# Optimization experiments

Measured on AMD Instinct MI355X. Metric: run time of the kernel, lower is better.

The kernel has to match this reference:

```python
import jax, jax.numpy as jnp
import numpy as np

B, IN_DIM, HID, LAT, L, K = 65536, 512, 256, 64, 3, 2048


def setup_inputs() -> dict:
    key = jax.random.key(0)
    ks = jax.random.split(key, 10)
    s = 0.05
    return {
        "x": jax.random.normal(ks[0], (B, IN_DIM), jnp.float32),
        "enc_w1": jax.random.normal(ks[1], (IN_DIM, HID), jnp.float32) * s,
        "enc_b1": jnp.zeros((HID,), jnp.float32),
        "enc_w2": jax.random.normal(ks[2], (HID, LAT), jnp.float32) * s,
        "enc_b2": jnp.zeros((LAT,), jnp.float32),
        "codebooks": jax.random.normal(ks[3], (L, K, LAT), jnp.float32),
        "dec_w1": jax.random.normal(ks[4], (LAT, HID), jnp.float32) * s,
        "dec_b1": jnp.zeros((HID,), jnp.float32),
        "dec_w2": jax.random.normal(ks[5], (HID, IN_DIM), jnp.float32) * s,
        "dec_b2": jnp.zeros((IN_DIM,), jnp.float32),
    }


def reference(x, enc_w1, enc_b1, enc_w2, enc_b2, codebooks,
              dec_w1, dec_b1, dec_w2, dec_b2):
    # encoder: Linear -> ReLU -> Linear
    z = jax.nn.relu(x @ enc_w1 + enc_b1) @ enc_w2 + enc_b2  # [B, LAT]

    quantized = jnp.zeros_like(z)
    codes, residuals = [], []
    num_layers = codebooks.shape[0]
    for i in range(num_layers):  # small fixed layer loop (structurally sequential)
        residual = z - jax.lax.stop_gradient(quantized)  # [B, LAT]
        residuals.append(residual)
        C = codebooks[i]  # [K, LAT]
        # squared euclidean distances (argmin identical to cdist argmin)
        sqdist = (jnp.sum(residual * residual, axis=-1, keepdims=True)
                  - 2.0 * (residual @ C.T)
                  + jnp.sum(C * C, axis=-1))  # [B, K]
        code = jnp.argmin(sqdist, axis=-1)  # [B]
        codes.append(code)
        quantized = C[code] + jax.lax.stop_gradient(quantized)

    # decoder: Linear -> ReLU -> Linear
    x_recon = jax.nn.relu(quantized @ dec_w1 + dec_b1) @ dec_w2 + dec_b2  # [B, IN_DIM]
    return (jnp.stack(codes), x_recon, quantized, jnp.stack(residuals))
```

## Files before the change

### kernel.cpp

```cpp
#include <hip/hip_runtime.h>
#include <float.h>

#define NB      65536
#define IN_DIM  512
#define HID     256
#define LAT     64
#define NLAYERS 3
#define NK      2048
#define DELTA   1e-2f

typedef __attribute__((ext_vector_type(8)))  short s16x8;
typedef __attribute__((ext_vector_type(16))) float fp32x16;

__device__ __forceinline__ unsigned short f2bf(float v) {
  unsigned u = __float_as_uint(v);
  unsigned r = (u + 0x7fffu + ((u >> 16) & 1u)) >> 16;
  return (unsigned short)r;
}
__device__ __forceinline__ float bf2f(unsigned short h) {
  return __uint_as_float((unsigned)h << 16);
}

template<bool RELU>
__global__ __launch_bounds__(256) void gemm_f32(
    const float* __restrict__ A, const float* __restrict__ W,
    const float* __restrict__ bias, float* __restrict__ C,
    int M, int N, int K) {
  __shared__ float As[32][132];
  __shared__ float Bs[32][64];
  const int tid = threadIdx.x;
  const int cg  = tid & 15;
  const int rg  = tid >> 4;
  const int m0  = blockIdx.x * 128;
  const int n0  = blockIdx.y * 64;

  float acc[8][4];
#pragma unroll
  for (int i = 0; i < 8; ++i)
#pragma unroll
    for (int j = 0; j < 4; ++j) acc[i][j] = 0.f;

  for (int k0 = 0; k0 < K; k0 += 32) {
#pragma unroll
    for (int p = 0; p < 4; ++p) {
      int a = tid + p * 256;
      int row = a >> 3, kq = (a & 7) * 4;
      float4 v = *reinterpret_cast<const float4*>(&A[(size_t)(m0 + row) * K + k0 + kq]);
      As[kq + 0][row] = v.x; As[kq + 1][row] = v.y;
      As[kq + 2][row] = v.z; As[kq + 3][row] = v.w;
    }
#pragma unroll
    for (int p = 0; p < 2; ++p) {
      int a = tid + p * 256;
      int kk = a >> 4, nq = (a & 15) * 4;
      *reinterpret_cast<float4*>(&Bs[kk][nq]) =
          *reinterpret_cast<const float4*>(&W[(size_t)(k0 + kk) * N + n0 + nq]);
    }
    __syncthreads();
#pragma unroll
    for (int kk = 0; kk < 32; ++kk) {
      float4 a0 = *reinterpret_cast<const float4*>(&As[kk][rg * 8]);
      float4 a1 = *reinterpret_cast<const float4*>(&As[kk][rg * 8 + 4]);
      float4 b0 = *reinterpret_cast<const float4*>(&Bs[kk][cg * 4]);
      float av[8] = {a0.x, a0.y, a0.z, a0.w, a1.x, a1.y, a1.z, a1.w};
      float bv[4] = {b0.x, b0.y, b0.z, b0.w};
#pragma unroll
      for (int i = 0; i < 8; ++i)
#pragma unroll
        for (int j = 0; j < 4; ++j)
          acc[i][j] = fmaf(av[i], bv[j], acc[i][j]);
    }
    __syncthreads();
  }

  float4 bb = *reinterpret_cast<const float4*>(&bias[n0 + cg * 4]);
  float bv[4] = {bb.x, bb.y, bb.z, bb.w};
#pragma unroll
  for (int i = 0; i < 8; ++i) {
    float vals[4];
#pragma unroll
    for (int j = 0; j < 4; ++j) {
      float v = __fadd_rn(acc[i][j], bv[j]);
      if (RELU) v = fmaxf(v, 0.f);
      vals[j] = v;
    }
    float4 o; o.x = vals[0]; o.y = vals[1]; o.z = vals[2]; o.w = vals[3];
    *reinterpret_cast<float4*>(&C[(size_t)(m0 + rg * 8 + i) * N + n0 + cg * 4]) = o;
  }
}

template<bool RELU>
__global__ __launch_bounds__(256) void gemm128(
    const float* __restrict__ A, const float* __restrict__ W,
    const float* __restrict__ bias, float* __restrict__ C,
    int M, int N, int K) {
  __shared__ float As[16][132];
  __shared__ float Bs[16][132];
  const int tid  = threadIdx.x;
  const int cg   = tid & 15;
  const int rg   = tid >> 4;
  const int sw   = (cg >> 2) & 1;
  const int colA = cg * 8 + sw * 4;
  const int colB = cg * 8 + (sw ^ 1) * 4;
  const int m0   = blockIdx.x * 128;
  const int n0   = blockIdx.y * 128;

  const int arow = tid >> 2;
  const int akq  = (tid & 3) * 4;
  const int bk   = tid >> 5;
  const int bn   = (tid & 31) * 4;

  const float* Ap0 = A + (size_t)(m0 + arow) * K + akq;
  const float* Ap1 = A + (size_t)(m0 + arow + 64) * K + akq;
  const float* Wp0 = W + (size_t)bk * N + n0 + bn;
  const float* Wp1 = W + (size_t)(bk + 8) * N + n0 + bn;

  float acc[8][8];
#pragma unroll
  for (int i = 0; i < 8; ++i)
#pragma unroll
    for (int j = 0; j < 8; ++j) acc[i][j] = 0.f;

  float4 av0, av1, bv0, bv1;
  av0 = *reinterpret_cast<const float4*>(Ap0);
  av1 = *reinterpret_cast<const float4*>(Ap1);
  bv0 = *reinterpret_cast<const float4*>(Wp0);
  bv1 = *reinterpret_cast<const float4*>(Wp1);

  auto write_tile = [&]() {
    As[akq + 0][arow] = av0.x; As[akq + 1][arow] = av0.y;
    As[akq + 2][arow] = av0.z; As[akq + 3][arow] = av0.w;
    As[akq + 0][arow + 64] = av1.x; As[akq + 1][arow + 64] = av1.y;
    As[akq + 2][arow + 64] = av1.z; As[akq + 3][arow + 64] = av1.w;
    *reinterpret_cast<float4*>(&Bs[bk][bn])     = bv0;
    *reinterpret_cast<float4*>(&Bs[bk + 8][bn]) = bv1;
  };
  auto compute_tile = [&]() {
#pragma unroll
    for (int kk = 0; kk < 16; ++kk) {
      float4 a0 = *reinterpret_cast<const float4*>(&As[kk][rg * 8]);
      float4 a1 = *reinterpret_cast<const float4*>(&As[kk][rg * 8 + 4]);
      float4 b0 = *reinterpret_cast<const float4*>(&Bs[kk][colA]);
      float4 b1 = *reinterpret_cast<const float4*>(&Bs[kk][colB]);
      float rv[8] = {a0.x, a0.y, a0.z, a0.w, a1.x, a1.y, a1.z, a1.w};
      float cv[8] = {b0.x, b0.y, b0.z, b0.w, b1.x, b1.y, b1.z, b1.w};
#pragma unroll
      for (int i = 0; i < 8; ++i)
#pragma unroll
        for (int j = 0; j < 8; ++j)
          acc[i][j] = fmaf(rv[i], cv[j], acc[i][j]);
    }
  };

  write_tile();
  __syncthreads();
#pragma unroll 1
  for (int k0 = 16; k0 < K; k0 += 16) {
    av0 = *reinterpret_cast<const float4*>(Ap0 + k0);
    av1 = *reinterpret_cast<const float4*>(Ap1 + k0);
    bv0 = *reinterpret_cast<const float4*>(Wp0 + (size_t)k0 * N);
    bv1 = *reinterpret_cast<const float4*>(Wp1 + (size_t)k0 * N);
    compute_tile();
    __syncthreads();
    write_tile();
    __syncthreads();
  }
  compute_tile();

  float4 bA = *reinterpret_cast<const float4*>(&bias[n0 + colA]);
  float4 bB = *reinterpret_cast<const float4*>(&bias[n0 + colB]);
  float ba[8] = {bA.x, bA.y, bA.z, bA.w, bB.x, bB.y, bB.z, bB.w};
#pragma unroll
  for (int i = 0; i < 8; ++i) {
    size_t row = (size_t)(m0 + rg * 8 + i);
    float o[8];
#pragma unroll
    for (int j = 0; j < 8; ++j) {
      float v = __fadd_rn(acc[i][j], ba[j]);
      if (RELU) v = fmaxf(v, 0.f);
      o[j] = v;
    }
    float4 oA; oA.x = o[0]; oA.y = o[1]; oA.z = o[2]; oA.w = o[3];
    float4 oB; oB.x = o[4]; oB.y = o[5]; oB.z = o[6]; oB.w = o[7];
    *reinterpret_cast<float4*>(&C[row * N + n0 + colA]) = oA;
    *reinterpret_cast<float4*>(&C[row * N + n0 + colB]) = oB;
  }
}

__global__ void cnorm_f32(const float* __restrict__ cb, float* __restrict__ cn) {
  int i = blockIdx.x * blockDim.x + threadIdx.x;
  if (i >= NLAYERS * NK) return;
  const float* row = cb + (size_t)i * LAT;
  float r[8];
#pragma unroll
  for (int j = 0; j < 8; ++j) r[j] = 0.f;
#pragma unroll
  for (int t = 0; t < 8; ++t)
#pragma unroll
    for (int j = 0; j < 8; ++j) {
      float v = row[t * 8 + j];
      r[j] = __fadd_rn(r[j], __fmul_rn(v, v));
    }
  cn[i] = __fadd_rn(__fadd_rn(__fadd_rn(r[0], r[1]), __fadd_rn(r[2], r[3])),
                    __fadd_rn(__fadd_rn(r[4], r[5]), __fadd_rn(r[6], r[7])));
}

__global__ void split_cb(const float* __restrict__ cb,
                         unsigned short* __restrict__ cbf) {
  const int sid  = blockIdx.x * 256 + threadIdx.x;
  const int lane = sid & 63;
  const int grp  = sid >> 6;
  const int fg   = grp & 7;
  const int chl  = grp >> 3;
  const int nt = fg >> 2, ks = fg & 3;
  const int layer = chl >> 5, ch = chl & 31;
  const int code = ch * 64 + nt * 32 + (lane & 31);
  const int k0 = ks * 16 + (lane >> 5) * 8;
  const float* src = cb + ((size_t)layer * NK + code) * LAT + k0;
  float4 a = *(const float4*)src;
  float4 b = *(const float4*)(src + 4);
  float v[8] = {a.x, a.y, a.z, a.w, b.x, b.y, b.z, b.w};
  s16x8 hi, lo;
#pragma unroll
  for (int i = 0; i < 8; ++i) {
    unsigned short h = f2bf(v[i]);
    hi[i] = (short)h;
    lo[i] = (short)f2bf(__fsub_rn(v[i], bf2f(h)));
  }
  *(s16x8*)(cbf + ((size_t)grp * 2 + 0) * 512 + lane * 8) = hi;
  *(s16x8*)(cbf + ((size_t)grp * 2 + 1) * 512 + lane * 8) = lo;
}

__global__ void split_w(const float* __restrict__ W,
                        unsigned short* __restrict__ wf, int K, int N) {
  const int total = (K / 16) * (N / 32) * 64;
  const int idx = blockIdx.x * 256 + threadIdx.x;
  if (idx >= total) return;
  const int lane = idx & 63;
  const int grp  = idx >> 6;
  const int ntn  = N / 32;
  const int ks   = grp / ntn;
  const int ntg  = grp % ntn;
  const int col  = ntg * 32 + (lane & 31);
  const int k0   = ks * 16 + (lane >> 5) * 8;
  s16x8 hi, lo;
#pragma unroll
  for (int i = 0; i < 8; ++i) {
    float v = W[(size_t)(k0 + i) * N + col];
    unsigned short h = f2bf(v);
    hi[i] = (short)h;
    lo[i] = (short)f2bf(__fsub_rn(v, bf2f(h)));
  }
  *(s16x8*)(wf + ((size_t)grp * 2 + 0) * 512 + lane * 8) = hi;
  *(s16x8*)(wf + ((size_t)grp * 2 + 1) * 512 + lane * 8) = lo;
}

__global__ __launch_bounds__(256, 2) void rq_mfma(
    const float* __restrict__ zg,
    const float* __restrict__ cb,
    const unsigned short* __restrict__ cbf,
    const float* __restrict__ cnorm,
    float* __restrict__ out_codes,
    float* __restrict__ out_quant,
    float* __restrict__ out_res) {
  __shared__ float m1S[64][4];
  __shared__ int   candS[64][16];
  __shared__ int   cntS[64][4];
  __shared__ int   flagS[64][4];
  __shared__ int   selS[64];
  __shared__ float rnS[64];
  __shared__ float bestD[256];
  __shared__ int   bestK[256];

  const int tid  = threadIdx.x;
  const int w    = tid >> 6;
  const int lane = tid & 63;
  const int half = lane >> 5;
  const int lcol = lane & 31;
  const int rb0  = blockIdx.x * 64;

  s16x8 ah[2][4], al[2][4];

  for (int layer = 0; layer < NLAYERS; ++layer) {
    const float* cbL = cb + (size_t)layer * NK * LAT;
    const float* cnL = cnorm + (size_t)layer * NK;
    const unsigned short* cbfL = cbf + (size_t)layer * (NK * LAT * 2);
    float* resL = out_res + (size_t)layer * NB * LAT;

#pragma unroll
    for (int m = 0; m < 2; ++m) {
      const size_t row = (size_t)(rb0 + m * 32 + lcol);
#pragma unroll
      for (int ks = 0; ks < 4; ++ks) {
        const int k0 = ks * 16 + half * 8;
        const float* zp = zg + row * LAT + k0;
        float4 a = *(const float4*)zp;
        float4 b = *(const float4*)(zp + 4);
        float r[8] = {a.x, a.y, a.z, a.w, b.x, b.y, b.z, b.w};
        if (layer > 0) {
          const float* qp = out_quant + row * LAT + k0;
          float4 qa = *(const float4*)qp;
          float4 qb = *(const float4*)(qp + 4);
          float q[8] = {qa.x, qa.y, qa.z, qa.w, qb.x, qb.y, qb.z, qb.w};
#pragma unroll
          for (int i = 0; i < 8; ++i) r[i] = __fsub_rn(r[i], q[i]);
          if (w == 0) {
            float4 o0 = {r[0], r[1], r[2], r[3]};
            float4 o1 = {r[4], r[5], r[6], r[7]};
            *(float4*)(resL + row * LAT + k0) = o0;
            *(float4*)(resL + row * LAT + k0 + 4) = o1;
          }
        }
#pragma unroll
        for (int i = 0; i < 8; ++i) {
          unsigned short hh = f2bf(r[i]);
          float hf = bf2f(hh);
          ah[m][ks][i] = (short)hh;
          al[m][ks][i] = (short)f2bf(__fsub_rn(r[i], hf));
        }
      }
    }
    __syncthreads();

    if (tid < 64) {
      const float* rp = resL + (size_t)(rb0 + tid) * LAT;
      float r8[8] = {0.f, 0.f, 0.f, 0.f, 0.f, 0.f, 0.f, 0.f};
#pragma unroll
      for (int tb = 0; tb < 8; ++tb) {
        float4 x0 = *(const float4*)(rp + tb * 8);
        float4 x1 = *(const float4*)(rp + tb * 8 + 4);
        float v[8] = {x0.x, x0.y, x0.z, x0.w, x1.x, x1.y, x1.z, x1.w};
#pragma unroll
        for (int j = 0; j < 8; ++j)
          r8[j] = __fadd_rn(r8[j], __fmul_rn(v[j], v[j]));
      }
      rnS[tid] = __fadd_rn(
          __fadd_rn(__fadd_rn(r8[0], r8[1]), __fadd_rn(r8[2], r8[3])),
          __fadd_rn(__fadd_rn(r8[4], r8[5]), __fadd_rn(r8[6], r8[7])));
    }

    float v1[2][16], v2[2][16];
    int   i1[2][16];
#pragma unroll
    for (int m = 0; m < 2; ++m)
#pragma unroll
      for (int r = 0; r < 16; ++r) {
        v1[m][r] = FLT_MAX; v2[m][r] = FLT_MAX; i1[m][r] = 0;
      }

#pragma unroll 1
    for (int ch = 0; ch < 8; ++ch) {
      const int chg = w * 8 + ch;
      const unsigned short* cf = cbfL + (size_t)chg * 8192;
#pragma unroll
      for (int nt = 0; nt < 2; ++nt) {
        const int kbase = chg * 64 + nt * 32 + lcol;
        float cnv = cnL[kbase];
        s16x8 bh[4], bl[4];
#pragma unroll
        for (int ks = 0; ks < 4; ++ks) {
          bh[ks] = *(const s16x8*)(cf + ((size_t)((nt * 4 + ks) * 2 + 0) * 64 + lane) * 8);
          bl[ks] = *(const s16x8*)(cf + ((size_t)((nt * 4 + ks) * 2 + 1) * 64 + lane) * 8);
        }
        fp32x16 acc0, acc1;
#pragma unroll
        for (int r = 0; r < 16; ++r) { acc0[r] = 0.f; acc1[r] = 0.f; }
#pragma unroll
        for (int ks = 0; ks < 4; ++ks) {
          acc0 = __builtin_amdgcn_mfma_f32_32x32x16_bf16(ah[0][ks], bh[ks], acc0, 0, 0, 0);
          acc1 = __builtin_amdgcn_mfma_f32_32x32x16_bf16(ah[1][ks], bh[ks], acc1, 0, 0, 0);
          acc0 = __builtin_amdgcn_mfma_f32_32x32x16_bf16(ah[0][ks], bl[ks], acc0, 0, 0, 0);
          acc1 = __builtin_amdgcn_mfma_f32_32x32x16_bf16(ah[1][ks], bl[ks], acc1, 0, 0, 0);
          acc0 = __builtin_amdgcn_mfma_f32_32x32x16_bf16(al[0][ks], bh[ks], acc0, 0, 0, 0);
          acc1 = __builtin_amdgcn_mfma_f32_32x32x16_bf16(al[1][ks], bh[ks], acc1, 0, 0, 0);
        }
#pragma unroll
        for (int r = 0; r < 16; ++r) {
          {
            float d = fmaf(-2.f, acc0[r], cnv);
            float t = fmaxf(d, v1[0][r]);
            v2[0][r] = fminf(v2[0][r], t);
            bool c = d < v1[0][r];
            i1[0][r] = c ? kbase : i1[0][r];
            v1[0][r] = fminf(v1[0][r], d);
          }
          {
            float d = fmaf(-2.f, acc1[r], cnv);
            float t = fmaxf(d, v1[1][r]);
            v2[1][r] = fminf(v2[1][r], t);
            bool c = d < v1[1][r];
            i1[1][r] = c ? kbase : i1[1][r];
            v1[1][r] = fminf(v1[1][r], d);
          }
        }
      }
    }

#pragma unroll
    for (int m = 0; m < 2; ++m)
#pragma unroll
      for (int r = 0; r < 16; ++r) {
        float m1 = v1[m][r];
        m1 = fminf(m1, __shfl_xor(m1, 1));
        m1 = fminf(m1, __shfl_xor(m1, 2));
        m1 = fminf(m1, __shfl_xor(m1, 4));
        m1 = fminf(m1, __shfl_xor(m1, 8));
        m1 = fminf(m1, __shfl_xor(m1, 16));
        const int rowloc = m * 32 + (r & 3) + 8 * (r >> 2) + 4 * half;
        if (lcol == 0) m1S[rowloc][w] = m1;
      }
    __syncthreads();
#pragma unroll
    for (int m = 0; m < 2; ++m)
#pragma unroll
      for (int r = 0; r < 16; ++r) {
        const int rowloc = m * 32 + (r & 3) + 8 * (r >> 2) + 4 * half;
        float thr = fminf(fminf(m1S[rowloc][0], m1S[rowloc][1]),
                          fminf(m1S[rowloc][2], m1S[rowloc][3])) + DELTA;
        unsigned long long bc = __ballot(v1[m][r] <= thr);
        unsigned long long bf = __ballot(v2[m][r] <= thr);
        unsigned mc = (unsigned)(bc >> (half * 32));
        unsigned mf = (unsigned)(bf >> (half * 32));
        int pos = __popc(mc & ((1u << lcol) - 1u));
        if (v1[m][r] <= thr && pos < 4) candS[rowloc][w * 4 + pos] = i1[m][r];
        if (lcol == 0) {
          int c = __popc(mc);
          cntS[rowloc][w]  = (c < 4) ? c : 4;
          flagS[rowloc][w] = (mf != 0u) || (c > 4);
        }
      }
    __syncthreads();

    if (tid < 64) {
      const int t = tid;
      if ((flagS[t][0] | flagS[t][1] | flagS[t][2] | flagS[t][3]) == 0) {
        const float* rp = resL + (size_t)(rb0 + t) * LAT;
        float rr[64];
#pragma unroll
        for (int j = 0; j < 16; ++j) {
          float4 x = *(const float4*)(rp + j * 4);
          rr[j * 4 + 0] = x.x; rr[j * 4 + 1] = x.y;
          rr[j * 4 + 2] = x.z; rr[j * 4 + 3] = x.w;
        }
        const float rn = rnS[t];
        float bd = FLT_MAX; int bk = 0x7fffffff;
#pragma unroll 1
        for (int w4 = 0; w4 < 4; ++w4) {
          const int cc = cntS[t][w4];
          for (int c = 0; c < cc; ++c) {
            int k = candS[t][w4 * 4 + c];
            const float* cp = cbL + (size_t)k * LAT;
            float dot = 0.f;
#pragma unroll
            for (int j = 0; j < 64; ++j) dot = fmaf(rr[j], cp[j], dot);
            float d = __fadd_rn(__fsub_rn(rn, __fmul_rn(2.f, dot)), cnL[k]);
            if (d < bd || (d == bd && k < bk)) { bd = d; bk = k; }
          }
        }
        selS[t] = bk;
        out_codes[(size_t)layer * NB + rb0 + t] = (float)bk;
      }
    }
    __syncthreads();

#pragma unroll 1
    for (int t2 = 0; t2 < 64; ++t2) {
      if ((flagS[t2][0] | flagS[t2][1] | flagS[t2][2] | flagS[t2][3]) == 0) continue;
      const float* rp = resL + (size_t)(rb0 + t2) * LAT;
      const float rn = rnS[t2];
      float bd = FLT_MAX; int bk = 0x7fffffff;
#pragma unroll 1
      for (int j = 0; j < 8; ++j) {
        int k = tid * 8 + j;
        const float* cp = cbL + (size_t)k * LAT;
        float dot = 0.f;
        for (int q = 0; q < 64; ++q) dot = fmaf(rp[q], cp[q], dot);
        float d = __fadd_rn(__fsub_rn(rn, __fmul_rn(2.f, dot)), cnL[k]);
        if (d < bd || (d == bd && k < bk)) { bd = d; bk = k; }
      }
      bestD[tid] = bd; bestK[tid] = bk;
      __syncthreads();
      if (tid == 0) {
        float gd = FLT_MAX; int gk = 0x7fffffff;
        for (int i = 0; i < 256; ++i) {
          float d = bestD[i]; int k = bestK[i];
          if (d < gd || (d == gd && k < gk)) { gd = d; gk = k; }
        }
        selS[t2] = gk;
        out_codes[(size_t)layer * NB + rb0 + t2] = (float)gk;
      }
      __syncthreads();
    }

    if (w < 2) {
      const int m = w;
      const int rowloc = m * 32 + lcol;
      const size_t row = (size_t)(rb0 + rowloc);
      const int sel = selS[rowloc];
      const float* cp = cbL + (size_t)sel * LAT;
#pragma unroll
      for (int ks = 0; ks < 4; ++ks) {
        const int k0 = ks * 16 + half * 8;
        float4 c0 = *(const float4*)(cp + k0);
        float4 c1 = *(const float4*)(cp + k0 + 4);
        float* qp = out_quant + row * LAT + k0;
        if (layer == 0) {
          *(float4*)qp = c0; *(float4*)(qp + 4) = c1;
        } else {
          float4 q0 = *(const float4*)qp;
          float4 q1 = *(const float4*)(qp + 4);
          q0.x = __fadd_rn(c0.x, q0.x); q0.y = __fadd_rn(c0.y, q0.y);
          q0.z = __fadd_rn(c0.z, q0.z); q0.w = __fadd_rn(c0.w, q0.w);
          q1.x = __fadd_rn(c1.x, q1.x); q1.y = __fadd_rn(c1.y, q1.y);
          q1.z = __fadd_rn(c1.z, q1.z); q1.w = __fadd_rn(c1.w, q1.w);
          *(float4*)qp = q0; *(float4*)(qp + 4) = q1;
        }
      }
    }
    __syncthreads();
  }
}

__global__ __launch_bounds__(256) void dec1_mfma(
    const float* __restrict__ q, const unsigned short* __restrict__ wf,
    const float* __restrict__ bias,
    unsigned short* __restrict__ h_hi, unsigned short* __restrict__ h_lo) {
  const int tid  = threadIdx.x;
  const int w    = tid >> 6;
  const int lane = tid & 63;
  const int half = lane >> 5;
  const int lcol = lane & 31;
  const int m0   = blockIdx.x * 128 + w * 32;
  const int n0   = blockIdx.y * 128;

  fp32x16 acc[4];
#pragma unroll
  for (int nt = 0; nt < 4; ++nt)
#pragma unroll
    for (int r = 0; r < 16; ++r) acc[nt][r] = 0.f;

  const size_t arow = (size_t)(m0 + lcol);
#pragma unroll
  for (int ks = 0; ks < 4; ++ks) {
    const float* ap = q + arow * LAT + ks * 16 + half * 8;
    float4 a0 = *(const float4*)ap;
    float4 a1 = *(const float4*)(ap + 4);
    float av[8] = {a0.x, a0.y, a0.z, a0.w, a1.x, a1.y, a1.z, a1.w};
    s16x8 ah, al;
#pragma unroll
    for (int i = 0; i < 8; ++i) {
      unsigned short hh = f2bf(av[i]);
      ah[i] = (short)hh;
      al[i] = (short)f2bf(__fsub_rn(av[i], bf2f(hh)));
    }
#pragma unroll
    for (int nt = 0; nt < 4; ++nt) {
      const int grp = ks * 8 + (blockIdx.y * 4 + nt);
      const unsigned short* base = wf + (size_t)grp * 1024;
      s16x8 bh = *(const s16x8*)(base + lane * 8);
      s16x8 bl = *(const s16x8*)(base + 512 + lane * 8);
      acc[nt] = __builtin_amdgcn_mfma_f32_32x32x16_bf16(ah, bh, acc[nt], 0, 0, 0);
      acc[nt] = __builtin_amdgcn_mfma_f32_32x32x16_bf16(ah, bl, acc[nt], 0, 0, 0);
      acc[nt] = __builtin_amdgcn_mfma_f32_32x32x16_bf16(al, bh, acc[nt], 0, 0, 0);
    }
  }

#pragma unroll
  for (int nt = 0; nt < 4; ++nt) {
    const int col = n0 + nt * 32 + lcol;
    const float b = bias[col];
#pragma unroll
    for (int r = 0; r < 16; ++r) {
      const int rowo = (r & 3) + 8 * (r >> 2) + 4 * half;
      const size_t grow = (size_t)(m0 + rowo);
      float v = fmaxf(__fadd_rn(acc[nt][r], b), 0.f);
      unsigned short hh = f2bf(v);
      h_hi[grow * HID + col] = hh;
      h_lo[grow * HID + col] = f2bf(__fsub_rn(v, bf2f(hh)));
    }
  }
}

__global__ __launch_bounds__(256) void dec2_mfma(
    const unsigned short* __restrict__ h_hi,
    const unsigned short* __restrict__ h_lo,
    const unsigned short* __restrict__ wf,
    const float* __restrict__ bias, float* __restrict__ C) {
  const int tid  = threadIdx.x;
  const int w    = tid >> 6;
  const int lane = tid & 63;
  const int half = lane >> 5;
  const int lcol = lane & 31;
  const int m0   = blockIdx.x * 128 + w * 32;
  const int n0   = blockIdx.y * 128;

  fp32x16 acc[4];
#pragma unroll
  for (int nt = 0; nt < 4; ++nt)
#pragma unroll
    for (int r = 0; r < 16; ++r) acc[nt][r] = 0.f;

  const size_t arow = (size_t)(m0 + lcol);
#pragma unroll 1
  for (int ks = 0; ks < 16; ++ks) {
    const size_t aoff = arow * HID + ks * 16 + half * 8;
    s16x8 ah = *(const s16x8*)(h_hi + aoff);
    s16x8 al = *(const s16x8*)(h_lo + aoff);
#pragma unroll
    for (int nt = 0; nt < 4; ++nt) {
      const int grp = ks * 16 + (blockIdx.y * 4 + nt);
      const unsigned short* base = wf + (size_t)grp * 1024;
      s16x8 bh = *(const s16x8*)(base + lane * 8);
      s16x8 bl = *(const s16x8*)(base + 512 + lane * 8);
      acc[nt] = __builtin_amdgcn_mfma_f32_32x32x16_bf16(ah, bh, acc[nt], 0, 0, 0);
      acc[nt] = __builtin_amdgcn_mfma_f32_32x32x16_bf16(ah, bl, acc[nt], 0, 0, 0);
      acc[nt] = __builtin_amdgcn_mfma_f32_32x32x16_bf16(al, bh, acc[nt], 0, 0, 0);
    }
  }

#pragma unroll
  for (int nt = 0; nt < 4; ++nt) {
    const int col = n0 + nt * 32 + lcol;
    const float b = bias[col];
#pragma unroll
    for (int r = 0; r < 16; ++r) {
      const int rowo = (r & 3) + 8 * (r >> 2) + 4 * half;
      C[(size_t)(m0 + rowo) * IN_DIM + col] = __fadd_rn(acc[nt][r], b);
    }
  }
}

extern "C" void kernel_launch(void* const* d_in, const int* in_sizes, int n_in,
                              void* d_out, int out_size, void* d_ws, size_t ws_size,
                              hipStream_t stream) {
  (void)in_sizes; (void)n_in; (void)out_size;
  const float* x   = (const float*)d_in[0];
  const float* ew1 = (const float*)d_in[1];
  const float* eb1 = (const float*)d_in[2];
  const float* ew2 = (const float*)d_in[3];
  const float* eb2 = (const float*)d_in[4];
  const float* cbk = (const float*)d_in[5];
  const float* dw1 = (const float*)d_in[6];
  const float* db1 = (const float*)d_in[7];
  const float* dw2 = (const float*)d_in[8];
  const float* db2 = (const float*)d_in[9];

  float* out     = (float*)d_out;
  float* o_codes = out;
  float* o_xrec  = out + (size_t)NLAYERS * NB;
  float* o_quant = o_xrec + (size_t)NB * IN_DIM;
  float* o_res   = o_quant + (size_t)NB * LAT;

  char* ws = (char*)d_ws;
  float* h            = (float*)ws;
  unsigned short* hhi = (unsigned short*)ws;
  unsigned short* hlo = (unsigned short*)(ws + (size_t)32 * 1024 * 1024);
  float* cn           = (float*)(ws + (size_t)64 * 1024 * 1024);
  unsigned short* w1f = (unsigned short*)(ws + (size_t)64 * 1024 * 1024 + 32768);
  unsigned short* w2f = (unsigned short*)(ws + (size_t)64 * 1024 * 1024 + 32768 + 65536);
  const size_t ws_need = (size_t)64 * 1024 * 1024 + 32768 + 65536 + 524288;
  const bool fast_dec = ws_size >= ws_need;

  unsigned short* cbf = (unsigned short*)(o_xrec + (size_t)16 * 1024 * 1024);

  cnorm_f32<<<(NLAYERS * NK + 255) / 256, 256, 0, stream>>>(cbk, cn);
  split_cb<<<192, 256, 0, stream>>>(cbk, cbf);
  if (fast_dec) {
    split_w<<<((LAT / 16) * (HID / 32) * 64 + 255) / 256, 256, 0, stream>>>(dw1, w1f, LAT, HID);
    split_w<<<((HID / 16) * (IN_DIM / 32) * 64 + 255) / 256, 256, 0, stream>>>(dw2, w2f, HID, IN_DIM);
  }
  gemm128<true ><<<dim3(NB / 128, HID / 128), 256, 0, stream>>>(x, ew1, eb1, h,     NB, HID, IN_DIM);
  gemm_f32<false><<<dim3(NB / 128, LAT / 64),  256, 0, stream>>>(h, ew2, eb2, o_res, NB, LAT, HID);
  rq_mfma<<<NB / 64, 256, 0, stream>>>(o_res, cbk, cbf, cn, o_codes, o_quant, o_res);
  if (fast_dec) {
    dec1_mfma<<<dim3(NB / 128, 2), 256, 0, stream>>>(o_quant, w1f, db1, hhi, hlo);
    dec2_mfma<<<dim3(NB / 128, 4), 256, 0, stream>>>(hhi, hlo, w2f, db2, o_xrec);
  } else {
    gemm128<true ><<<dim3(NB / 128, HID / 128),    256, 0, stream>>>(o_quant, dw1, db1, h,      NB, HID,    LAT);
    gemm128<false><<<dim3(NB / 128, IN_DIM / 128), 256, 0, stream>>>(h,       dw2, db2, o_xrec, NB, IN_DIM, HID);
  }
}
```

Before: 800.3 us.

## Stage codebook chunks in LDS with double buffering, double rows per block

The residual-quantization kernel now handles 128 rows per block. Each pair of waves shares a 64-row group and splits every 64-code chunk between its two waves. The bf16-split codebook chunks and codebook norms are staged into double-buffered shared memory with register prefetch, instead of every wave loading its own codebook slice from global memory. This cuts global/L2 codebook traffic per row and overlaps the next chunk's load with MFMA work, at the cost of about 40KB of LDS, a block barrier per chunk, and half as many blocks.

Result: faster. 694.1 us (-13.3%).

```diff
diff --git a/kernel.cpp b/kernel.cpp
--- a/kernel.cpp
+++ b/kernel.cpp
@@ -263,21 +263,25 @@
     float* __restrict__ out_codes,
     float* __restrict__ out_quant,
     float* __restrict__ out_res) {
-  __shared__ float m1S[64][4];
-  __shared__ int   candS[64][16];
-  __shared__ int   cntS[64][4];
-  __shared__ int   flagS[64][4];
-  __shared__ int   selS[64];
-  __shared__ float rnS[64];
+  __shared__ unsigned short cbS[2][8192];
+  __shared__ float cnSL[NK];
+  __shared__ float m1S[128][2];
+  __shared__ int   candS[128][8];
+  __shared__ int   cntS[128][2];
+  __shared__ int   flagS[128][2];
+  __shared__ int   selS[128];
+  __shared__ float rnS[128];
   __shared__ float bestD[256];
   __shared__ int   bestK[256];
 
-  const int tid  = threadIdx.x;
-  const int w    = tid >> 6;
-  const int lane = tid & 63;
-  const int half = lane >> 5;
-  const int lcol = lane & 31;
-  const int rb0  = blockIdx.x * 64;
+  const int tid    = threadIdx.x;
+  const int w      = tid >> 6;
+  const int rgrp   = w >> 1;
+  const int nthalf = w & 1;
+  const int lane   = tid & 63;
+  const int half   = lane >> 5;
+  const int lcol   = lane & 31;
+  const int rb0    = blockIdx.x * 128;
 
   s16x8 ah[2][4], al[2][4];
 
@@ -289,7 +293,7 @@
 
 #pragma unroll
     for (int m = 0; m < 2; ++m) {
-      const size_t row = (size_t)(rb0 + m * 32 + lcol);
+      const size_t row = (size_t)(rb0 + rgrp * 64 + m * 32 + lcol);
 #pragma unroll
       for (int ks = 0; ks < 4; ++ks) {
         const int k0 = ks * 16 + half * 8;
@@ -304,7 +308,7 @@
           float q[8] = {qa.x, qa.y, qa.z, qa.w, qb.x, qb.y, qb.z, qb.w};
 #pragma unroll
           for (int i = 0; i < 8; ++i) r[i] = __fsub_rn(r[i], q[i]);
-          if (w == 0) {
+          if (nthalf == 0) {
             float4 o0 = {r[0], r[1], r[2], r[3]};
             float4 o1 = {r[4], r[5], r[6], r[7]};
             *(float4*)(resL + row * LAT + k0) = o0;
@@ -320,9 +324,21 @@
         }
       }
     }
-    __syncthreads();
-
-    if (tid < 64) {
+
+    s16x8 stg[4];
+#pragma unroll
+    for (int p = 0; p < 4; ++p)
+      stg[p] = *(const s16x8*)(cbfL + p * 2048 + tid * 8);
+    float4 cn0 = *(const float4*)(cnL + tid * 8);
+    float4 cn1 = *(const float4*)(cnL + tid * 8 + 4);
+    __syncthreads();
+
+#pragma unroll
+    for (int p = 0; p < 4; ++p)
+      *(s16x8*)(&cbS[0][p * 2048 + tid * 8]) = stg[p];
+    *(float4*)(&cnSL[tid * 8])     = cn0;
+    *(float4*)(&cnSL[tid * 8 + 4]) = cn1;
+    if (tid < 128) {
       const float* rp = resL + (size_t)(rb0 + tid) * LAT;
       float r8[8] = {0.f, 0.f, 0.f, 0.f, 0.f, 0.f, 0.f, 0.f};
 #pragma unroll
@@ -338,6 +354,7 @@
           __fadd_rn(__fadd_rn(r8[0], r8[1]), __fadd_rn(r8[2], r8[3])),
           __fadd_rn(__fadd_rn(r8[4], r8[5]), __fadd_rn(r8[6], r8[7])));
     }
+    __syncthreads();
 
     float v1[2][16], v2[2][16];
     int   i1[2][16];
@@ -349,51 +366,64 @@
       }
 
 #pragma unroll 1
-    for (int ch = 0; ch < 8; ++ch) {
-      const int chg = w * 8 + ch;
-      const unsigned short* cf = cbfL + (size_t)chg * 8192;
-#pragma unroll
-      for (int nt = 0; nt < 2; ++nt) {
-        const int kbase = chg * 64 + nt * 32 + lcol;
-        float cnv = cnL[kbase];
-        s16x8 bh[4], bl[4];
-#pragma unroll
-        for (int ks = 0; ks < 4; ++ks) {
-          bh[ks] = *(const s16x8*)(cf + ((size_t)((nt * 4 + ks) * 2 + 0) * 64 + lane) * 8);
-          bl[ks] = *(const s16x8*)(cf + ((size_t)((nt * 4 + ks) * 2 + 1) * 64 + lane) * 8);
-        }
-        fp32x16 acc0, acc1;
-#pragma unroll
-        for (int r = 0; r < 16; ++r) { acc0[r] = 0.f; acc1[r] = 0.f; }
-#pragma unroll
-        for (int ks = 0; ks < 4; ++ks) {
-          acc0 = __builtin_amdgcn_mfma_f32_32x32x16_bf16(ah[0][ks], bh[ks], acc0, 0, 0, 0);
-          acc1 = __builtin_amdgcn_mfma_f32_32x32x16_bf16(ah[1][ks], bh[ks], acc1, 0, 0, 0);
-          acc0 = __builtin_amdgcn_mfma_f32_32x32x16_bf16(ah[0][ks], bl[ks], acc0, 0, 0, 0);
-          acc1 = __builtin_amdgcn_mfma_f32_32x32x16_bf16(ah[1][ks], bl[ks], acc1, 0, 0, 0);
-          acc0 = __builtin_amdgcn_mfma_f32_32x32x16_bf16(al[0][ks], bh[ks], acc0, 0, 0, 0);
-          acc1 = __builtin_amdgcn_mfma_f32_32x32x16_bf16(al[1][ks], bh[ks], acc1, 0, 0, 0);
-        }
-#pragma unroll
-        for (int r = 0; r < 16; ++r) {
-          {
-            float d = fmaf(-2.f, acc0[r], cnv);
-            float t = fmaxf(d, v1[0][r]);
-            v2[0][r] = fminf(v2[0][r], t);
-            bool c = d < v1[0][r];
-            i1[0][r] = c ? kbase : i1[0][r];
-            v1[0][r] = fminf(v1[0][r], d);
-          }
-          {
-            float d = fmaf(-2.f, acc1[r], cnv);
-            float t = fmaxf(d, v1[1][r]);
-            v2[1][r] = fminf(v2[1][r], t);
-            bool c = d < v1[1][r];
-            i1[1][r] = c ? kbase : i1[1][r];
-            v1[1][r] = fminf(v1[1][r], d);
-          }
-        }
-      }
+    for (int ch = 0; ch < 32; ++ch) {
+      const int buf = ch & 1;
+      const bool haveNext = (ch + 1) < 32;
+      if (haveNext) {
+        const unsigned short* src = cbfL + (size_t)(ch + 1) * 8192;
+#pragma unroll
+        for (int p = 0; p < 4; ++p)
+          stg[p] = *(const s16x8*)(src + p * 2048 + tid * 8);
+      }
+
+      s16x8 bh[4], bl[4];
+#pragma unroll
+      for (int ks = 0; ks < 4; ++ks) {
+        bh[ks] = *(const s16x8*)(&cbS[buf][((nthalf * 4 + ks) * 2 + 0) * 512 + lane * 8]);
+        bl[ks] = *(const s16x8*)(&cbS[buf][((nthalf * 4 + ks) * 2 + 1) * 512 + lane * 8]);
+      }
+      const int kbase = ch * 64 + nthalf * 32 + lcol;
+      const float cnv = cnSL[kbase];
+
+      fp32x16 acc0, acc1;
+#pragma unroll
+      for (int r = 0; r < 16; ++r) { acc0[r] = 0.f; acc1[r] = 0.f; }
+#pragma unroll
+      for (int ks = 0; ks < 4; ++ks) {
+        acc0 = __builtin_amdgcn_mfma_f32_32x32x16_bf16(ah[0][ks], bh[ks], acc0, 0, 0, 0);
+        acc1 = __builtin_amdgcn_mfma_f32_32x32x16_bf16(ah[1][ks], bh[ks], acc1, 0, 0, 0);
+        acc0 = __builtin_amdgcn_mfma_f32_32x32x16_bf16(ah[0][ks], bl[ks], acc0, 0, 0, 0);
+        acc1 = __builtin_amdgcn_mfma_f32_32x32x16_bf16(ah[1][ks], bl[ks], acc1, 0, 0, 0);
+        acc0 = __builtin_amdgcn_mfma_f32_32x32x16_bf16(al[0][ks], bh[ks], acc0, 0, 0, 0);
+        acc1 = __builtin_amdgcn_mfma_f32_32x32x16_bf16(al[1][ks], bh[ks], acc1, 0, 0, 0);
+      }
+
+#pragma unroll
+      for (int r = 0; r < 16; ++r) {
+        {
+          float d = fmaf(-2.f, acc0[r], cnv);
+          float nv2 = fminf(fmaxf(d, v1[0][r]), v2[0][r]);
+          bool c = d < v1[0][r];
+          i1[0][r] = c ? kbase : i1[0][r];
+          v1[0][r] = fminf(v1[0][r], d);
+          v2[0][r] = nv2;
+        }
+        {
+          float d = fmaf(-2.f, acc1[r], cnv);
+          float nv2 = fminf(fmaxf(d, v1[1][r]), v2[1][r]);
+          bool c = d < v1[1][r];
+          i1[1][r] = c ? kbase : i1[1][r];
+          v1[1][r] = fminf(v1[1][r], d);
+          v2[1][r] = nv2;
+        }
+      }
+
+      if (haveNext) {
+#pragma unroll
+        for (int p = 0; p < 4; ++p)
+          *(s16x8*)(&cbS[buf ^ 1][p * 2048 + tid * 8]) = stg[p];
+      }
+      __syncthreads();
     }
 
 #pragma unroll
@@ -406,34 +436,33 @@
         m1 = fminf(m1, __shfl_xor(m1, 4));
         m1 = fminf(m1, __shfl_xor(m1, 8));
         m1 = fminf(m1, __shfl_xor(m1, 16));
-        const int rowloc = m * 32 + (r & 3) + 8 * (r >> 2) + 4 * half;
-        if (lcol == 0) m1S[rowloc][w] = m1;
+        const int rowloc = rgrp * 64 + m * 32 + (r & 3) + 8 * (r >> 2) + 4 * half;
+        if (lcol == 0) m1S[rowloc][nthalf] = m1;
       }
     __syncthreads();
 #pragma unroll
     for (int m = 0; m < 2; ++m)
 #pragma unroll
       for (int r = 0; r < 16; ++r) {
-        const int rowloc = m * 32 + (r & 3) + 8 * (r >> 2) + 4 * half;
-        float thr = fminf(fminf(m1S[rowloc][0], m1S[rowloc][1]),
-                          fminf(m1S[rowloc][2], m1S[rowloc][3])) + DELTA;
+        const int rowloc = rgrp * 64 + m * 32 + (r & 3) + 8 * (r >> 2) + 4 * half;
+        float thr = fminf(m1S[rowloc][0], m1S[rowloc][1]) + DELTA;
         unsigned long long bc = __ballot(v1[m][r] <= thr);
         unsigned long long bf = __ballot(v2[m][r] <= thr);
         unsigned mc = (unsigned)(bc >> (half * 32));
         unsigned mf = (unsigned)(bf >> (half * 32));
         int pos = __popc(mc & ((1u << lcol) - 1u));
-        if (v1[m][r] <= thr && pos < 4) candS[rowloc][w * 4 + pos] = i1[m][r];
+        if (v1[m][r] <= thr && pos < 4) candS[rowloc][nthalf * 4 + pos] = i1[m][r];
         if (lcol == 0) {
           int c = __popc(mc);
-          cntS[rowloc][w]  = (c < 4) ? c : 4;
-          flagS[rowloc][w] = (mf != 0u) || (c > 4);
-        }
-      }
-    __syncthreads();
-
-    if (tid < 64) {
+          cntS[rowloc][nthalf]  = (c < 4) ? c : 4;
+          flagS[rowloc][nthalf] = (mf != 0u) || (c > 4);
+        }
+      }
+    __syncthreads();
+
+    if (tid < 128) {
       const int t = tid;
-      if ((flagS[t][0] | flagS[t][1] | flagS[t][2] | flagS[t][3]) == 0) {
+      if ((flagS[t][0] | flagS[t][1]) == 0) {
         const float* rp = resL + (size_t)(rb0 + t) * LAT;
         float rr[64];
 #pragma unroll
@@ -444,18 +473,15 @@
         }
         const float rn = rnS[t];
         float bd = FLT_MAX; int bk = 0x7fffffff;
-#pragma unroll 1
-        for (int w4 = 0; w4 < 4; ++w4) {
-          const int cc = cntS[t][w4];
-          for (int c = 0; c < cc; ++c) {
-            int k = candS[t][w4 * 4 + c];
-            const float* cp = cbL + (size_t)k * LAT;
-            float dot = 0.f;
-#pragma unroll
-            for (int j = 0; j < 64; ++j) dot = fmaf(rr[j], cp[j], dot);
-            float d = __fadd_rn(__fsub_rn(rn, __fmul_rn(2.f, dot)), cnL[k]);
-            if (d < bd || (d == bd && k < bk)) { bd = d; bk = k; }
-          }
+        const int c0 = cntS[t][0], c1n = cntS[t][1];
+        for (int c = 0; c < c0 + c1n; ++c) {
+          int k = candS[t][(c < c0) ? c : (4 + c - c0)];
+          const float* cp = cbL + (size_t)k * LAT;
+          float dot = 0.f;
+#pragma unroll
+          for (int j = 0; j < 64; ++j) dot = fmaf(rr[j], cp[j], dot);
+          float d = __fadd_rn(__fsub_rn(rn, __fmul_rn(2.f, dot)), cnL[k]);
+          if (d < bd || (d == bd && k < bk)) { bd = d; bk = k; }
         }
         selS[t] = bk;
         out_codes[(size_t)layer * NB + rb0 + t] = (float)bk;
@@ -464,8 +490,8 @@
     __syncthreads();
 
 #pragma unroll 1
-    for (int t2 = 0; t2 < 64; ++t2) {
-      if ((flagS[t2][0] | flagS[t2][1] | flagS[t2][2] | flagS[t2][3]) == 0) continue;
+    for (int t2 = 0; t2 < 128; ++t2) {
+      if ((flagS[t2][0] | flagS[t2][1]) == 0) continue;
       const float* rp = resL + (size_t)(rb0 + t2) * LAT;
       const float rn = rnS[t2];
       float bd = FLT_MAX; int bk = 0x7fffffff;
@@ -492,28 +518,30 @@
       __syncthreads();
     }
 
-    if (w < 2) {
-      const int m = w;
-      const int rowloc = m * 32 + lcol;
-      const size_t row = (size_t)(rb0 + rowloc);
-      const int sel = selS[rowloc];
-      const float* cp = cbL + (size_t)sel * LAT;
-#pragma unroll
-      for (int ks = 0; ks < 4; ++ks) {
-        const int k0 = ks * 16 + half * 8;
-        float4 c0 = *(const float4*)(cp + k0);
-        float4 c1 = *(const float4*)(cp + k0 + 4);
-        float* qp = out_quant + row * LAT + k0;
-        if (layer == 0) {
-          *(float4*)qp = c0; *(float4*)(qp + 4) = c1;
-        } else {
-          float4 q0 = *(const float4*)qp;
-          float4 q1 = *(const float4*)(qp + 4);
-          q0.x = __fadd_rn(c0.x, q0.x); q0.y = __fadd_rn(c0.y, q0.y);
-          q0.z = __fadd_rn(c0.z, q0.z); q0.w = __fadd_rn(c0.w, q0.w);
-          q1.x = __fadd_rn(c1.x, q1.x); q1.y = __fadd_rn(c1.y, q1.y);
-          q1.z = __fadd_rn(c1.z, q1.z); q1.w = __fadd_rn(c1.w, q1.w);
-          *(float4*)qp = q0; *(float4*)(qp + 4) = q1;
+    if (nthalf == 0) {
+#pragma unroll
+      for (int m = 0; m < 2; ++m) {
+        const int rowloc = rgrp * 64 + m * 32 + lcol;
+        const size_t row = (size_t)(rb0 + rowloc);
+        const int sel = selS[rowloc];
+        const float* cp = cbL + (size_t)sel * LAT;
+#pragma unroll
+        for (int ks = 0; ks < 4; ++ks) {
+          const int k0 = ks * 16 + half * 8;
+          float4 c0 = *(const float4*)(cp + k0);
+          float4 c1 = *(const float4*)(cp + k0 + 4);
+          float* qp = out_quant + row * LAT + k0;
+          if (layer == 0) {
+            *(float4*)qp = c0; *(float4*)(qp + 4) = c1;
+          } else {
+            float4 q0 = *(const float4*)qp;
+            float4 q1 = *(const float4*)(qp + 4);
+            q0.x = __fadd_rn(c0.x, q0.x); q0.y = __fadd_rn(c0.y, q0.y);
+            q0.z = __fadd_rn(c0.z, q0.z); q0.w = __fadd_rn(c0.w, q0.w);
+            q1.x = __fadd_rn(c1.x, q1.x); q1.y = __fadd_rn(c1.y, q1.y);
+            q1.z = __fadd_rn(c1.z, q1.z); q1.w = __fadd_rn(c1.w, q1.w);
+            *(float4*)qp = q0; *(float4*)(qp + 4) = q1;
+          }
         }
       }
     }
@@ -671,7 +699,7 @@
   }
   gemm128<true ><<<dim3(NB / 128, HID / 128), 256, 0, stream>>>(x, ew1, eb1, h,     NB, HID, IN_DIM);
   gemm_f32<false><<<dim3(NB / 128, LAT / 64),  256, 0, stream>>>(h, ew2, eb2, o_res, NB, LAT, HID);
-  rq_mfma<<<NB / 64, 256, 0, stream>>>(o_res, cbk, cbf, cn, o_codes, o_quant, o_res);
+  rq_mfma<<<NB / 128, 256, 0, stream>>>(o_res, cbk, cbf, cn, o_codes, o_quant, o_res);
   if (fast_dec) {
     dec1_mfma<<<dim3(NB / 128, 2), 256, 0, stream>>>(o_quant, w1f, db1, hhi, hlo);
     dec2_mfma<<<dim3(NB / 128, 4), 256, 0, stream>>>(hhi, hlo, w2f, db2, o_xrec);
```
